# Kernel tuning notes

Hardware: AMD Instinct MI355X
Metric: run time of the kernel (lower is better)

The kernel has to match this reference:

```python
import jax, jax.numpy as jnp
import numpy as np

BATCH = 1024
SEQ = 80
VOCAB = 50000
EMB = 512
UNITS = 512


def setup_inputs() -> dict:
    key = jax.random.key(0)
    ks = jax.random.split(key, 10)
    s_in = 1.0 / np.sqrt(EMB)
    s_h = 1.0 / np.sqrt(UNITS)
    return {
        "inputs": jax.random.randint(ks[0], (BATCH, SEQ), 0, VOCAB, dtype=jnp.int64),
        "emb": jax.random.normal(ks[1], (VOCAB, EMB), dtype=jnp.float32) * 0.05,
        "W0x": jax.random.normal(ks[2], (EMB, UNITS), dtype=jnp.float32) * s_in,
        "W0h": jax.random.normal(ks[3], (UNITS, UNITS), dtype=jnp.float32) * s_h,
        "b0": jnp.zeros((UNITS,), dtype=jnp.float32),
        "W1x": jax.random.normal(ks[4], (UNITS, UNITS), dtype=jnp.float32) * s_h,
        "W1h": jax.random.normal(ks[5], (UNITS, UNITS), dtype=jnp.float32) * s_h,
        "b1": jnp.zeros((UNITS,), dtype=jnp.float32),
        "Wout": jax.random.normal(ks[6], (UNITS, 1), dtype=jnp.float32) * s_h,
        "bout": jnp.zeros((1,), dtype=jnp.float32),
    }


def reference(inputs, emb, W0x, W0h, b0, W1x, W1h, b1, Wout, bout):
    # Embedding lookup: [B, T, E]
    x = emb[inputs]
    # Time-major for scan: [T, B, E]
    xs = jnp.transpose(x, (1, 0, 2))

    h0 = jnp.zeros((inputs.shape[0], W0h.shape[0]), dtype=emb.dtype)
    h1 = jnp.zeros((inputs.shape[0], W1h.shape[0]), dtype=emb.dtype)

    def step(carry, x_t):
        h0, h1 = carry
        # SimpleRNNCell 0: tanh(x@Wx + h@Wh + b)  (dropout inactive at inference)
        h0 = jnp.tanh(x_t @ W0x + h0 @ W0h + b0)
        # SimpleRNNCell 1 stacked on cell 0's output
        h1 = jnp.tanh(h0 @ W1x + h1 @ W1h + b1)
        return (h0, h1), None

    (h0, h1), _ = jax.lax.scan(step, (h0, h1), xs)
    # Dense(1) on last-step hidden of layer 1, then sigmoid -> [B, 1]
    prob = jax.nn.sigmoid(h1 @ Wout + bout)
    return prob
```

## Files before the change

### kernel.cpp

```cpp
#include <hip/hip_runtime.h>
#include <hip/hip_bf16.h>
#include <math.h>

#define BATCH   1024
#define SEQ     80
#define EMB     512
#define UNITS   512
#define NBG     64
#define NCG     4
#define ROWS    16
#define COLS    128
#define THREADS 512
#define LDW     1544

#define H0_OFF   (2u * 1024 * 1024)
#define H1_OFF   (4u * 1024 * 1024)
#define FLAG_OFF (6u * 1024 * 1024)

typedef __attribute__((ext_vector_type(8))) short          bf16x8;
typedef __attribute__((ext_vector_type(8))) unsigned short u16x8;
typedef __attribute__((ext_vector_type(4))) float          f32x4;

__device__ inline unsigned short f2bf(float f) {
    __hip_bfloat16 h = __float2bfloat16(f);
    return *reinterpret_cast<unsigned short*>(&h);
}
__device__ inline float bf2f(unsigned short u) {
    unsigned int x = ((unsigned int)u) << 16;
    return __uint_as_float(x);
}
__device__ inline float tanh_fast(float x) {
    float e = __expf(2.f * x);
    return 1.f - 2.f / (e + 1.f);
}

__global__ __launch_bounds__(256) void pack_weights(
    const float* __restrict__ W0x, const float* __restrict__ W0h,
    const float* __restrict__ W1x, const float* __restrict__ W1h,
    unsigned short* __restrict__ wpack)
{
    int g    = blockIdx.x * 4 + (threadIdx.x >> 6);
    int lane = threadIdx.x & 63;
    int p    = g >> 10;
    int cg   = (g >> 8) & 3;
    int w    = (g >> 5) & 7;
    int k0   = g & 31;
    int n    = cg * COLS + w * 16 + (lane & 15);
    int kb   = k0 * 32 + (lane >> 4) * 8;
    const float* Wx = p ? W1x : W0x;
    const float* Wh = p ? W1h : W0h;

    u16x8 v;
#pragma unroll
    for (int j = 0; j < 8; ++j) {
        int k = kb + j;
        float f = (k < 512) ? Wx[(size_t)k * UNITS + n]
                            : Wh[(size_t)(k - 512) * UNITS + n];
        v[j] = f2bf(f);
    }
    *(u16x8*)(wpack + (size_t)g * 512 + lane * 8) = v;
}

#define RUN_PHASE(ACC, KBASE, WB)                                              \
    do {                                                                       \
        const unsigned short* a_lds = hcat + abase + (KBASE);                  \
        bf16x8 Bf[8];                                                          \
        _Pragma("unroll")                                                      \
        for (int i = 0; i < 8; ++i)                                            \
            Bf[i] = *(const bf16x8*)((WB) + (size_t)i * 512);                  \
        _Pragma("unroll")                                                      \
        for (int k0 = 0; k0 < 32; ++k0) {                                      \
            bf16x8 a = *(const bf16x8*)(a_lds + k0 * 32);                      \
            bf16x8 b = Bf[k0 & 7];                                             \
            if (k0 + 8 < 32)                                                   \
                Bf[k0 & 7] = *(const bf16x8*)((WB) + (size_t)(k0 + 8) * 512);  \
            ACC = __builtin_amdgcn_mfma_f32_16x16x32_bf16(a, b, ACC, 0, 0, 0); \
        }                                                                      \
    } while (0)

__global__ __launch_bounds__(THREADS, 1) void rnn_ex_kernel(
    const int*   __restrict__ inputs,
    const float* __restrict__ emb,
    const float* __restrict__ b0,
    const float* __restrict__ b1,
    const unsigned short* __restrict__ wpack,
    unsigned short* __restrict__ h0buf,
    unsigned short* __restrict__ h1buf,
    int* __restrict__ flag0,
    int* __restrict__ flag1,
    const float* __restrict__ Wout,
    const float* __restrict__ bout,
    float*       __restrict__ out)
{
    __shared__ unsigned short hcat[ROWS * LDW];

    const int tid   = threadIdx.x;
    const int w     = tid >> 6;
    const int lane  = tid & 63;
    const int quad  = lane >> 4;
    const int l15   = lane & 15;
    const int cg    = blockIdx.x >> 6;
    const int bg    = blockIdx.x & 63;
    const int rbase = bg * ROWS;

    for (int i = tid; i < ROWS * 1024; i += THREADS) {
        int r = i >> 10, c = i & 1023;
        hcat[r * LDW + 512 + c] = 0;
    }

    const int xr = tid >> 5;
    const int xc = (tid & 31) * 16;

    {
        int idx = inputs[(rbase + xr) * SEQ + 0];
        const float4* ep = (const float4*)(emb + (size_t)idx * EMB + xc);
        float4 p0 = ep[0], p1 = ep[1], p2 = ep[2], p3 = ep[3];
        u16x8 v0, v1;
        v0[0]=f2bf(p0.x); v0[1]=f2bf(p0.y); v0[2]=f2bf(p0.z); v0[3]=f2bf(p0.w);
        v0[4]=f2bf(p1.x); v0[5]=f2bf(p1.y); v0[6]=f2bf(p1.z); v0[7]=f2bf(p1.w);
        v1[0]=f2bf(p2.x); v1[1]=f2bf(p2.y); v1[2]=f2bf(p2.z); v1[3]=f2bf(p2.w);
        v1[4]=f2bf(p3.x); v1[5]=f2bf(p3.y); v1[6]=f2bf(p3.z); v1[7]=f2bf(p3.w);
        *(u16x8*)(hcat + xr * LDW + xc)     = v0;
        *(u16x8*)(hcat + xr * LDW + xc + 8) = v1;
    }
    __syncthreads();

    const int   mycol = cg * COLS + w * 16 + l15;
    const float bias0 = b0[mycol];
    const float bias1 = b1[mycol];

    const unsigned short* wb0 = wpack + ((size_t)(cg * 256 + w * 32)) * 512 + lane * 8;
    const unsigned short* wb1 = wb0 + (size_t)1024 * 512;

    const int abase = l15 * LDW + quad * 8;
    const int fl    = bg * NCG;

    for (int t = 0; t < SEQ; ++t) {
        const int par = t & 1;
        const int tgt = t + 1;

        int tn = (t + 1 < SEQ) ? t + 1 : t;
        int idx = inputs[(rbase + xr) * SEQ + tn];
        const float4* ep = (const float4*)(emb + (size_t)idx * EMB + xc);
        float4 p0 = ep[0], p1 = ep[1], p2 = ep[2], p3 = ep[3];

        f32x4 acc = {bias0, bias0, bias0, bias0};
        RUN_PHASE(acc, 0, wb0);
        {
            unsigned short* dst = h0buf +
                ((size_t)par * BATCH + rbase + quad * 4) * UNITS + mycol;
#pragma unroll
            for (int i = 0; i < 4; ++i)
                __hip_atomic_store(dst + (size_t)i * UNITS,
                                   f2bf(tanh_fast(acc[i])),
                                   __ATOMIC_RELAXED, __HIP_MEMORY_SCOPE_AGENT);
        }
        __syncthreads();
        if (tid == 0)
            __hip_atomic_store(&flag0[fl + cg], tgt,
                               __ATOMIC_RELEASE, __HIP_MEMORY_SCOPE_AGENT);
        if (tid < NCG)
            while (__hip_atomic_load(&flag0[fl + tid],
                                     __ATOMIC_RELAXED, __HIP_MEMORY_SCOPE_AGENT) < tgt)
                __builtin_amdgcn_s_sleep(1);
        __asm__ volatile("" ::: "memory");
        __syncthreads();
        {
            const unsigned long long* src = (const unsigned long long*)
                (h0buf + ((size_t)par * BATCH + rbase) * UNITS);
            int base = (xr * 512 + xc) >> 2;
            unsigned long long q0 = __hip_atomic_load(src + base + 0, __ATOMIC_RELAXED, __HIP_MEMORY_SCOPE_AGENT);
            unsigned long long q1 = __hip_atomic_load(src + base + 1, __ATOMIC_RELAXED, __HIP_MEMORY_SCOPE_AGENT);
            unsigned long long q2 = __hip_atomic_load(src + base + 2, __ATOMIC_RELAXED, __HIP_MEMORY_SCOPE_AGENT);
            unsigned long long q3 = __hip_atomic_load(src + base + 3, __ATOMIC_RELAXED, __HIP_MEMORY_SCOPE_AGENT);
            unsigned long long* d = (unsigned long long*)&hcat[xr * LDW + 512 + xc];
            d[0] = q0; d[1] = q1; d[2] = q2; d[3] = q3;

            u16x8 v0, v1;
            v0[0]=f2bf(p0.x); v0[1]=f2bf(p0.y); v0[2]=f2bf(p0.z); v0[3]=f2bf(p0.w);
            v0[4]=f2bf(p1.x); v0[5]=f2bf(p1.y); v0[6]=f2bf(p1.z); v0[7]=f2bf(p1.w);
            v1[0]=f2bf(p2.x); v1[1]=f2bf(p2.y); v1[2]=f2bf(p2.z); v1[3]=f2bf(p2.w);
            v1[4]=f2bf(p3.x); v1[5]=f2bf(p3.y); v1[6]=f2bf(p3.z); v1[7]=f2bf(p3.w);
            *(u16x8*)(hcat + xr * LDW + xc)     = v0;
            *(u16x8*)(hcat + xr * LDW + xc + 8) = v1;
        }
        __syncthreads();

        f32x4 acc2 = {bias1, bias1, bias1, bias1};
        RUN_PHASE(acc2, 512, wb1);
        {
            unsigned short* dst = h1buf +
                ((size_t)par * BATCH + rbase + quad * 4) * UNITS + mycol;
#pragma unroll
            for (int i = 0; i < 4; ++i)
                __hip_atomic_store(dst + (size_t)i * UNITS,
                                   f2bf(tanh_fast(acc2[i])),
                                   __ATOMIC_RELAXED, __HIP_MEMORY_SCOPE_AGENT);
        }
        __syncthreads();
        if (tid == 0)
            __hip_atomic_store(&flag1[fl + cg], tgt,
                               __ATOMIC_RELEASE, __HIP_MEMORY_SCOPE_AGENT);
        if (tid < NCG)
            while (__hip_atomic_load(&flag1[fl + tid],
                                     __ATOMIC_RELAXED, __HIP_MEMORY_SCOPE_AGENT) < tgt)
                __builtin_amdgcn_s_sleep(1);
        __asm__ volatile("" ::: "memory");
        __syncthreads();
        {
            const unsigned long long* src = (const unsigned long long*)
                (h1buf + ((size_t)par * BATCH + rbase) * UNITS);
            int base = (xr * 512 + xc) >> 2;
            unsigned long long q0 = __hip_atomic_load(src + base + 0, __ATOMIC_RELAXED, __HIP_MEMORY_SCOPE_AGENT);
            unsigned long long q1 = __hip_atomic_load(src + base + 1, __ATOMIC_RELAXED, __HIP_MEMORY_SCOPE_AGENT);
            unsigned long long q2 = __hip_atomic_load(src + base + 2, __ATOMIC_RELAXED, __HIP_MEMORY_SCOPE_AGENT);
            unsigned long long q3 = __hip_atomic_load(src + base + 3, __ATOMIC_RELAXED, __HIP_MEMORY_SCOPE_AGENT);
            unsigned long long* d = (unsigned long long*)&hcat[xr * LDW + 1024 + xc];
            d[0] = q0; d[1] = q1; d[2] = q2; d[3] = q3;
        }
    }
    __syncthreads();

    if (cg == 0) {
#pragma unroll
        for (int rr = 0; rr < 2; ++rr) {
            int r = w * 2 + rr;
            float s = 0.f;
#pragma unroll
            for (int j = 0; j < 8; ++j) {
                int c = lane + 64 * j;
                s += bf2f(hcat[r * LDW + 1024 + c]) * Wout[c];
            }
#pragma unroll
            for (int off = 32; off > 0; off >>= 1) s += __shfl_down(s, off);
            if (lane == 0) {
                float z = s + bout[0];
                out[rbase + r] = 1.f / (1.f + __expf(-z));
            }
        }
    }
}

extern "C" void kernel_launch(void* const* d_in, const int* in_sizes, int n_in,
                              void* d_out, int out_size, void* d_ws, size_t ws_size,
                              hipStream_t stream) {
    const int*   inputs = (const int*)d_in[0];
    const float* emb    = (const float*)d_in[1];
    const float* W0x    = (const float*)d_in[2];
    const float* W0h    = (const float*)d_in[3];
    const float* b0     = (const float*)d_in[4];
    const float* W1x    = (const float*)d_in[5];
    const float* W1h    = (const float*)d_in[6];
    const float* b1     = (const float*)d_in[7];
    const float* Wout   = (const float*)d_in[8];
    const float* bout   = (const float*)d_in[9];
    float*       out    = (float*)d_out;

    unsigned short* wpack = (unsigned short*)d_ws;
    unsigned short* h0buf = (unsigned short*)((char*)d_ws + H0_OFF);
    unsigned short* h1buf = (unsigned short*)((char*)d_ws + H1_OFF);
    int* flag0 = (int*)((char*)d_ws + FLAG_OFF);
    int* flag1 = flag0 + 256;

    hipMemsetAsync((char*)d_ws + FLAG_OFF, 0, 2048, stream);
    pack_weights<<<512, 256, 0, stream>>>(W0x, W0h, W1x, W1h, wpack);
    rnn_ex_kernel<<<NBG * NCG, THREADS, 0, stream>>>(
        inputs, emb, b0, b1, wpack, h0buf, h1buf, flag0, flag1,
        Wout, bout, out);
}
```

Before: 1.103 ms.

## Pipeline RNN as four producer/consumer stages over ring buffers per batch group

Splits the work by matrix instead of by output column: four block groups each own one of W0x, W0h, W1x, W1h, all 512 output columns. The input projection (stage 0) and the layer-1 input projection (stage 2) are taken off the recurrent critical path and pass results through 5-deep global ring buffers guarded by flags. The recurrent stages keep h in double-buffered LDS, so no cross-block exchange of h slices is needed. The cost is extra global traffic for fp32 partial sums, more flag polling, and a serial chain of dependent stages whose latency may still bound throughput.

Result: slower. 1.700 ms (+54.2%).

```diff
diff --git a/kernel.cpp b/kernel.cpp
--- a/kernel.cpp
+++ b/kernel.cpp
@@ -7,19 +7,15 @@
 #define EMB     512
 #define UNITS   512
 #define NBG     64
-#define NCG     4
 #define ROWS    16
-#define COLS    128
 #define THREADS 512
-#define LDW     1544
-
-#define H0_OFF   (2u * 1024 * 1024)
-#define H1_OFF   (4u * 1024 * 1024)
-#define FLAG_OFF (6u * 1024 * 1024)
-
-typedef __attribute__((ext_vector_type(8))) short          bf16x8;
-typedef __attribute__((ext_vector_type(8))) unsigned short u16x8;
-typedef __attribute__((ext_vector_type(4))) float          f32x4;
+#define RING    5
+#define LDH     520
+
+typedef __attribute__((ext_vector_type(8))) short              bf16x8;
+typedef __attribute__((ext_vector_type(8))) unsigned short     u16x8;
+typedef __attribute__((ext_vector_type(4))) float              f32x4;
+typedef __attribute__((ext_vector_type(2))) unsigned long long u64x2;
 
 __device__ inline unsigned short f2bf(float f) {
     __hip_bfloat16 h = __float2bfloat16(f);
@@ -32,6 +28,27 @@
 __device__ inline float tanh_fast(float x) {
     float e = __expf(2.f * x);
     return 1.f - 2.f / (e + 1.f);
+}
+__device__ inline u16x8 pack8(float4 p0, float4 p1) {
+    u16x8 v;
+    v[0]=f2bf(p0.x); v[1]=f2bf(p0.y); v[2]=f2bf(p0.z); v[3]=f2bf(p0.w);
+    v[4]=f2bf(p1.x); v[5]=f2bf(p1.y); v[6]=f2bf(p1.z); v[7]=f2bf(p1.w);
+    return v;
+}
+__device__ inline void st_f32(float* p, float v) {
+    __hip_atomic_store(p, v, __ATOMIC_RELAXED, __HIP_MEMORY_SCOPE_AGENT);
+}
+__device__ inline void st_u16(unsigned short* p, unsigned short v) {
+    __hip_atomic_store(p, v, __ATOMIC_RELAXED, __HIP_MEMORY_SCOPE_AGENT);
+}
+__device__ inline float ld_f32(const float* p) {
+    return __hip_atomic_load(p, __ATOMIC_RELAXED, __HIP_MEMORY_SCOPE_AGENT);
+}
+__device__ inline unsigned long long ld_u64(const unsigned long long* p) {
+    return __hip_atomic_load(p, __ATOMIC_RELAXED, __HIP_MEMORY_SCOPE_AGENT);
+}
+__device__ inline int ld_flag(const int* p) {
+    return __hip_atomic_load(p, __ATOMIC_RELAXED, __HIP_MEMORY_SCOPE_AGENT);
 }
 
 __global__ __launch_bounds__(256) void pack_weights(
@@ -41,187 +58,260 @@
 {
     int g    = blockIdx.x * 4 + (threadIdx.x >> 6);
     int lane = threadIdx.x & 63;
-    int p    = g >> 10;
-    int cg   = (g >> 8) & 3;
-    int w    = (g >> 5) & 7;
-    int k0   = g & 31;
-    int n    = cg * COLS + w * 16 + (lane & 15);
-    int kb   = k0 * 32 + (lane >> 4) * 8;
-    const float* Wx = p ? W1x : W0x;
-    const float* Wh = p ? W1h : W0h;
+    int m    = g >> 9;
+    int w    = (g >> 6) & 7;
+    int nt   = (g >> 4) & 3;
+    int k    = g & 15;
+    int col  = w * 64 + nt * 16 + (lane & 15);
+    int rowb = k * 32 + (lane >> 4) * 8;
+    const float* src = (m == 0) ? W0x : (m == 1) ? W0h : (m == 2) ? W1x : W1h;
 
     u16x8 v;
 #pragma unroll
-    for (int j = 0; j < 8; ++j) {
-        int k = kb + j;
-        float f = (k < 512) ? Wx[(size_t)k * UNITS + n]
-                            : Wh[(size_t)(k - 512) * UNITS + n];
-        v[j] = f2bf(f);
-    }
+    for (int j = 0; j < 8; ++j)
+        v[j] = f2bf(src[(size_t)(rowb + j) * UNITS + col]);
     *(u16x8*)(wpack + (size_t)g * 512 + lane * 8) = v;
 }
 
-#define RUN_PHASE(ACC, KBASE, WB)                                              \
+#define NT_GEMM(ACC, WN)                                                       \
     do {                                                                       \
-        const unsigned short* a_lds = hcat + abase + (KBASE);                  \
-        bf16x8 Bf[8];                                                          \
+        bf16x8 Bf_[8];                                                         \
         _Pragma("unroll")                                                      \
-        for (int i = 0; i < 8; ++i)                                            \
-            Bf[i] = *(const bf16x8*)((WB) + (size_t)i * 512);                  \
+        for (int i_ = 0; i_ < 8; ++i_)                                         \
+            Bf_[i_] = *(const bf16x8*)((WN) + (size_t)i_ * 512);               \
         _Pragma("unroll")                                                      \
-        for (int k0 = 0; k0 < 32; ++k0) {                                      \
-            bf16x8 a = *(const bf16x8*)(a_lds + k0 * 32);                      \
-            bf16x8 b = Bf[k0 & 7];                                             \
-            if (k0 + 8 < 32)                                                   \
-                Bf[k0 & 7] = *(const bf16x8*)((WB) + (size_t)(k0 + 8) * 512);  \
-            ACC = __builtin_amdgcn_mfma_f32_16x16x32_bf16(a, b, ACC, 0, 0, 0); \
+        for (int k_ = 0; k_ < 16; ++k_) {                                      \
+            bf16x8 b_ = Bf_[k_ & 7];                                           \
+            if (k_ + 8 < 16)                                                   \
+                Bf_[k_ & 7] = *(const bf16x8*)((WN) + (size_t)(k_ + 8) * 512); \
+            ACC = __builtin_amdgcn_mfma_f32_16x16x32_bf16(av[k_], b_, ACC,     \
+                                                          0, 0, 0);            \
         }                                                                      \
     } while (0)
 
-__global__ __launch_bounds__(THREADS, 1) void rnn_ex_kernel(
+__global__ __launch_bounds__(THREADS, 2) void rnn_pipe(
     const int*   __restrict__ inputs,
     const float* __restrict__ emb,
     const float* __restrict__ b0,
     const float* __restrict__ b1,
     const unsigned short* __restrict__ wpack,
-    unsigned short* __restrict__ h0buf,
-    unsigned short* __restrict__ h1buf,
-    int* __restrict__ flag0,
-    int* __restrict__ flag1,
+    float*          __restrict__ pxring,
+    unsigned short* __restrict__ h0ring,
+    float*          __restrict__ uring,
+    int*            __restrict__ flg,
     const float* __restrict__ Wout,
     const float* __restrict__ bout,
     float*       __restrict__ out)
 {
-    __shared__ unsigned short hcat[ROWS * LDW];
+    __shared__ __align__(16) unsigned short sA[2 * ROWS * LDH];
 
     const int tid   = threadIdx.x;
     const int w     = tid >> 6;
     const int lane  = tid & 63;
     const int quad  = lane >> 4;
     const int l15   = lane & 15;
-    const int cg    = blockIdx.x >> 6;
+    const int stage = blockIdx.x >> 6;
     const int bg    = blockIdx.x & 63;
     const int rbase = bg * ROWS;
 
-    for (int i = tid; i < ROWS * 1024; i += THREADS) {
-        int r = i >> 10, c = i & 1023;
-        hcat[r * LDW + 512 + c] = 0;
-    }
-
-    const int xr = tid >> 5;
-    const int xc = (tid & 31) * 16;
-
-    {
-        int idx = inputs[(rbase + xr) * SEQ + 0];
-        const float4* ep = (const float4*)(emb + (size_t)idx * EMB + xc);
-        float4 p0 = ep[0], p1 = ep[1], p2 = ep[2], p3 = ep[3];
-        u16x8 v0, v1;
-        v0[0]=f2bf(p0.x); v0[1]=f2bf(p0.y); v0[2]=f2bf(p0.z); v0[3]=f2bf(p0.w);
-        v0[4]=f2bf(p1.x); v0[5]=f2bf(p1.y); v0[6]=f2bf(p1.z); v0[7]=f2bf(p1.w);
-        v1[0]=f2bf(p2.x); v1[1]=f2bf(p2.y); v1[2]=f2bf(p2.z); v1[3]=f2bf(p2.w);
-        v1[4]=f2bf(p3.x); v1[5]=f2bf(p3.y); v1[6]=f2bf(p3.z); v1[7]=f2bf(p3.w);
-        *(u16x8*)(hcat + xr * LDW + xc)     = v0;
-        *(u16x8*)(hcat + xr * LDW + xc + 8) = v1;
-    }
-    __syncthreads();
-
-    const int   mycol = cg * COLS + w * 16 + l15;
-    const float bias0 = b0[mycol];
-    const float bias1 = b1[mycol];
-
-    const unsigned short* wb0 = wpack + ((size_t)(cg * 256 + w * 32)) * 512 + lane * 8;
-    const unsigned short* wb1 = wb0 + (size_t)1024 * 512;
-
-    const int abase = l15 * LDW + quad * 8;
-    const int fl    = bg * NCG;
-
-    for (int t = 0; t < SEQ; ++t) {
-        const int par = t & 1;
-        const int tgt = t + 1;
-
-        int tn = (t + 1 < SEQ) ? t + 1 : t;
-        int idx = inputs[(rbase + xr) * SEQ + tn];
-        const float4* ep = (const float4*)(emb + (size_t)idx * EMB + xc);
-        float4 p0 = ep[0], p1 = ep[1], p2 = ep[2], p3 = ep[3];
-
-        f32x4 acc = {bias0, bias0, bias0, bias0};
-        RUN_PHASE(acc, 0, wb0);
-        {
-            unsigned short* dst = h0buf +
-                ((size_t)par * BATCH + rbase + quad * 4) * UNITS + mycol;
-#pragma unroll
-            for (int i = 0; i < 4; ++i)
-                __hip_atomic_store(dst + (size_t)i * UNITS,
-                                   f2bf(tanh_fast(acc[i])),
-                                   __ATOMIC_RELAXED, __HIP_MEMORY_SCOPE_AGENT);
+    const int gr   = w;
+    const int gc   = lane * 8;
+    const int aoff = l15 * LDH + quad * 8;
+    const int col0 = w * 64 + l15;
+
+    int* Fpx = flg;
+    int* Fh0 = flg + 64;
+    int* Fu  = flg + 128;
+    int* Fh1 = flg + 192;
+
+    const unsigned short* wb = wpack + ((size_t)((stage * 8 + w) * 64)) * 512
+                                     + lane * 8;
+
+    if (stage == 0) {
+        float bb[4];
+#pragma unroll
+        for (int nt = 0; nt < 4; ++nt) bb[nt] = b0[col0 + nt * 16];
+
+        for (int t = 0; t < SEQ; ++t) {
+            if (tid == 0)
+                while (ld_flag(&Fh0[bg]) < t - (RING - 1))
+                    __builtin_amdgcn_s_sleep(1);
+            __asm__ volatile("" ::: "memory");
+            __syncthreads();
+            if (tid == 0)
+                __hip_atomic_store(&Fpx[bg], t, __ATOMIC_RELEASE,
+                                   __HIP_MEMORY_SCOPE_AGENT);
+            {
+                int ia = inputs[(rbase + gr) * SEQ + t];
+                int ib = inputs[(rbase + gr + 8) * SEQ + t];
+                const float4* ea = (const float4*)(emb + (size_t)ia * EMB + gc);
+                const float4* eb = (const float4*)(emb + (size_t)ib * EMB + gc);
+                float4 f0 = ea[0], f1 = ea[1], f2 = eb[0], f3 = eb[1];
+                *(u16x8*)(sA + gr * LDH + gc)       = pack8(f0, f1);
+                *(u16x8*)(sA + (gr + 8) * LDH + gc) = pack8(f2, f3);
+            }
+            __syncthreads();
+
+            bf16x8 av[16];
+            const unsigned short* ar = sA + aoff;
+#pragma unroll
+            for (int k = 0; k < 16; ++k) av[k] = *(const bf16x8*)(ar + k * 32);
+
+            f32x4 acc[4];
+#pragma unroll
+            for (int nt = 0; nt < 4; ++nt) {
+                acc[nt] = (f32x4){bb[nt], bb[nt], bb[nt], bb[nt]};
+                NT_GEMM(acc[nt], wb + (size_t)(nt * 16) * 512);
+            }
+            float* dst = pxring + ((size_t)(t % RING) * NBG + bg) * 8192;
+#pragma unroll
+            for (int nt = 0; nt < 4; ++nt)
+#pragma unroll
+                for (int i = 0; i < 4; ++i)
+                    st_f32(dst + (quad * 4 + i) * 512 + col0 + nt * 16,
+                           acc[nt][i]);
         }
         __syncthreads();
         if (tid == 0)
-            __hip_atomic_store(&flag0[fl + cg], tgt,
-                               __ATOMIC_RELEASE, __HIP_MEMORY_SCOPE_AGENT);
-        if (tid < NCG)
-            while (__hip_atomic_load(&flag0[fl + tid],
-                                     __ATOMIC_RELAXED, __HIP_MEMORY_SCOPE_AGENT) < tgt)
-                __builtin_amdgcn_s_sleep(1);
-        __asm__ volatile("" ::: "memory");
-        __syncthreads();
-        {
-            const unsigned long long* src = (const unsigned long long*)
-                (h0buf + ((size_t)par * BATCH + rbase) * UNITS);
-            int base = (xr * 512 + xc) >> 2;
-            unsigned long long q0 = __hip_atomic_load(src + base + 0, __ATOMIC_RELAXED, __HIP_MEMORY_SCOPE_AGENT);
-            unsigned long long q1 = __hip_atomic_load(src + base + 1, __ATOMIC_RELAXED, __HIP_MEMORY_SCOPE_AGENT);
-            unsigned long long q2 = __hip_atomic_load(src + base + 2, __ATOMIC_RELAXED, __HIP_MEMORY_SCOPE_AGENT);
-            unsigned long long q3 = __hip_atomic_load(src + base + 3, __ATOMIC_RELAXED, __HIP_MEMORY_SCOPE_AGENT);
-            unsigned long long* d = (unsigned long long*)&hcat[xr * LDW + 512 + xc];
-            d[0] = q0; d[1] = q1; d[2] = q2; d[3] = q3;
-
-            u16x8 v0, v1;
-            v0[0]=f2bf(p0.x); v0[1]=f2bf(p0.y); v0[2]=f2bf(p0.z); v0[3]=f2bf(p0.w);
-            v0[4]=f2bf(p1.x); v0[5]=f2bf(p1.y); v0[6]=f2bf(p1.z); v0[7]=f2bf(p1.w);
-            v1[0]=f2bf(p2.x); v1[1]=f2bf(p2.y); v1[2]=f2bf(p2.z); v1[3]=f2bf(p2.w);
-            v1[4]=f2bf(p3.x); v1[5]=f2bf(p3.y); v1[6]=f2bf(p3.z); v1[7]=f2bf(p3.w);
-            *(u16x8*)(hcat + xr * LDW + xc)     = v0;
-            *(u16x8*)(hcat + xr * LDW + xc + 8) = v1;
-        }
-        __syncthreads();
-
-        f32x4 acc2 = {bias1, bias1, bias1, bias1};
-        RUN_PHASE(acc2, 512, wb1);
-        {
-            unsigned short* dst = h1buf +
-                ((size_t)par * BATCH + rbase + quad * 4) * UNITS + mycol;
-#pragma unroll
-            for (int i = 0; i < 4; ++i)
-                __hip_atomic_store(dst + (size_t)i * UNITS,
-                                   f2bf(tanh_fast(acc2[i])),
-                                   __ATOMIC_RELAXED, __HIP_MEMORY_SCOPE_AGENT);
+            __hip_atomic_store(&Fpx[bg], SEQ + 1, __ATOMIC_RELEASE,
+                               __HIP_MEMORY_SCOPE_AGENT);
+
+    } else if (stage == 1) {
+        for (int i = tid; i < ROWS * LDH; i += THREADS)
+            sA[ROWS * LDH + i] = 0;
+
+        for (int t = 0; t < SEQ; ++t) {
+            const int par = t & 1, slot = t % RING;
+            if (tid == 0) {
+                while (ld_flag(&Fu[bg])  < t - (RING - 1)) __builtin_amdgcn_s_sleep(1);
+                while (ld_flag(&Fpx[bg]) < t + 1)          __builtin_amdgcn_s_sleep(1);
+            }
+            __asm__ volatile("" ::: "memory");
+            __syncthreads();
+            if (tid == 0)
+                __hip_atomic_store(&Fh0[bg], t, __ATOMIC_RELEASE,
+                                   __HIP_MEMORY_SCOPE_AGENT);
+            const float* ps = pxring + ((size_t)slot * NBG + bg) * 8192;
+            f32x4 acc[4];
+#pragma unroll
+            for (int nt = 0; nt < 4; ++nt)
+#pragma unroll
+                for (int i = 0; i < 4; ++i)
+                    acc[nt][i] = ld_f32(ps + (quad * 4 + i) * 512 + col0 + nt * 16);
+
+            bf16x8 av[16];
+            const unsigned short* ar = sA + (par ^ 1) * ROWS * LDH + aoff;
+#pragma unroll
+            for (int k = 0; k < 16; ++k) av[k] = *(const bf16x8*)(ar + k * 32);
+#pragma unroll
+            for (int nt = 0; nt < 4; ++nt)
+                NT_GEMM(acc[nt], wb + (size_t)(nt * 16) * 512);
+
+            unsigned short* hd = sA + par * ROWS * LDH;
+            unsigned short* rs = h0ring + ((size_t)slot * NBG + bg) * 8192;
+#pragma unroll
+            for (int nt = 0; nt < 4; ++nt)
+#pragma unroll
+                for (int i = 0; i < 4; ++i) {
+                    unsigned short hv = f2bf(tanh_fast(acc[nt][i]));
+                    hd[(quad * 4 + i) * LDH + col0 + nt * 16] = hv;
+                    st_u16(rs + (quad * 4 + i) * 512 + col0 + nt * 16, hv);
+                }
         }
         __syncthreads();
         if (tid == 0)
-            __hip_atomic_store(&flag1[fl + cg], tgt,
-                               __ATOMIC_RELEASE, __HIP_MEMORY_SCOPE_AGENT);
-        if (tid < NCG)
-            while (__hip_atomic_load(&flag1[fl + tid],
-                                     __ATOMIC_RELAXED, __HIP_MEMORY_SCOPE_AGENT) < tgt)
-                __builtin_amdgcn_s_sleep(1);
-        __asm__ volatile("" ::: "memory");
+            __hip_atomic_store(&Fh0[bg], SEQ + 1, __ATOMIC_RELEASE,
+                               __HIP_MEMORY_SCOPE_AGENT);
+
+    } else if (stage == 2) {
+        float bb[4];
+#pragma unroll
+        for (int nt = 0; nt < 4; ++nt) bb[nt] = b1[col0 + nt * 16];
+
+        for (int t = 0; t < SEQ; ++t) {
+            const int slot = t % RING;
+            if (tid == 0) {
+                while (ld_flag(&Fh1[bg]) < t - (RING - 1)) __builtin_amdgcn_s_sleep(1);
+                while (ld_flag(&Fh0[bg]) < t + 1)          __builtin_amdgcn_s_sleep(1);
+            }
+            __asm__ volatile("" ::: "memory");
+            __syncthreads();
+            if (tid == 0)
+                __hip_atomic_store(&Fu[bg], t, __ATOMIC_RELEASE,
+                                   __HIP_MEMORY_SCOPE_AGENT);
+            const unsigned long long* hs = (const unsigned long long*)
+                (h0ring + ((size_t)slot * NBG + bg) * 8192);
+            bf16x8 av[16];
+#pragma unroll
+            for (int k = 0; k < 16; ++k) {
+                int eo = l15 * 512 + k * 32 + quad * 8;
+                u64x2 q;
+                q[0] = ld_u64(hs + (eo >> 2));
+                q[1] = ld_u64(hs + (eo >> 2) + 1);
+                av[k] = *(bf16x8*)&q;
+            }
+            f32x4 acc[4];
+#pragma unroll
+            for (int nt = 0; nt < 4; ++nt) {
+                acc[nt] = (f32x4){bb[nt], bb[nt], bb[nt], bb[nt]};
+                NT_GEMM(acc[nt], wb + (size_t)(nt * 16) * 512);
+            }
+            float* dst = uring + ((size_t)slot * NBG + bg) * 8192;
+#pragma unroll
+            for (int nt = 0; nt < 4; ++nt)
+#pragma unroll
+                for (int i = 0; i < 4; ++i)
+                    st_f32(dst + (quad * 4 + i) * 512 + col0 + nt * 16,
+                           acc[nt][i]);
+        }
         __syncthreads();
-        {
-            const unsigned long long* src = (const unsigned long long*)
-                (h1buf + ((size_t)par * BATCH + rbase) * UNITS);
-            int base = (xr * 512 + xc) >> 2;
-            unsigned long long q0 = __hip_atomic_load(src + base + 0, __ATOMIC_RELAXED, __HIP_MEMORY_SCOPE_AGENT);
-            unsigned long long q1 = __hip_atomic_load(src + base + 1, __ATOMIC_RELAXED, __HIP_MEMORY_SCOPE_AGENT);
-            unsigned long long q2 = __hip_atomic_load(src + base + 2, __ATOMIC_RELAXED, __HIP_MEMORY_SCOPE_AGENT);
-            unsigned long long q3 = __hip_atomic_load(src + base + 3, __ATOMIC_RELAXED, __HIP_MEMORY_SCOPE_AGENT);
-            unsigned long long* d = (unsigned long long*)&hcat[xr * LDW + 1024 + xc];
-            d[0] = q0; d[1] = q1; d[2] = q2; d[3] = q3;
-        }
-    }
-    __syncthreads();
-
-    if (cg == 0) {
+        if (tid == 0)
+            __hip_atomic_store(&Fu[bg], SEQ + 1, __ATOMIC_RELEASE,
+                               __HIP_MEMORY_SCOPE_AGENT);
+
+    } else {
+        for (int i = tid; i < ROWS * LDH; i += THREADS)
+            sA[ROWS * LDH + i] = 0;
+
+        for (int t = 0; t < SEQ; ++t) {
+            const int par = t & 1, slot = t % RING;
+            if (tid == 0)
+                while (ld_flag(&Fu[bg]) < t + 1) __builtin_amdgcn_s_sleep(1);
+            __asm__ volatile("" ::: "memory");
+            __syncthreads();
+            if (tid == 0)
+                __hip_atomic_store(&Fh1[bg], t, __ATOMIC_RELEASE,
+                                   __HIP_MEMORY_SCOPE_AGENT);
+            const float* us = uring + ((size_t)slot * NBG + bg) * 8192;
+            f32x4 acc[4];
+#pragma unroll
+            for (int nt = 0; nt < 4; ++nt)
+#pragma unroll
+                for (int i = 0; i < 4; ++i)
+                    acc[nt][i] = ld_f32(us + (quad * 4 + i) * 512 + col0 + nt * 16);
+
+            bf16x8 av[16];
+            const unsigned short* ar = sA + (par ^ 1) * ROWS * LDH + aoff;
+#pragma unroll
+            for (int k = 0; k < 16; ++k) av[k] = *(const bf16x8*)(ar + k * 32);
+#pragma unroll
+            for (int nt = 0; nt < 4; ++nt)
+                NT_GEMM(acc[nt], wb + (size_t)(nt * 16) * 512);
+
+            unsigned short* hd = sA + par * ROWS * LDH;
+#pragma unroll
+            for (int nt = 0; nt < 4; ++nt)
+#pragma unroll
+                for (int i = 0; i < 4; ++i)
+                    hd[(quad * 4 + i) * LDH + col0 + nt * 16] =
+                        f2bf(tanh_fast(acc[nt][i]));
+        }
+        __syncthreads();
+        if (tid == 0)
+            __hip_atomic_store(&Fh1[bg], SEQ + 1, __ATOMIC_RELEASE,
+                               __HIP_MEMORY_SCOPE_AGENT);
+
+        const unsigned short* h1l = sA + ((SEQ - 1) & 1) * ROWS * LDH;
 #pragma unroll
         for (int rr = 0; rr < 2; ++rr) {
             int r = w * 2 + rr;
@@ -229,7 +319,7 @@
 #pragma unroll
             for (int j = 0; j < 8; ++j) {
                 int c = lane + 64 * j;
-                s += bf2f(hcat[r * LDW + 1024 + c]) * Wout[c];
+                s += bf2f(h1l[r * LDH + c]) * Wout[c];
             }
 #pragma unroll
             for (int off = 32; off > 0; off >>= 1) s += __shfl_down(s, off);
@@ -256,15 +346,22 @@
     const float* bout   = (const float*)d_in[9];
     float*       out    = (float*)d_out;
 
-    unsigned short* wpack = (unsigned short*)d_ws;
-    unsigned short* h0buf = (unsigned short*)((char*)d_ws + H0_OFF);
-    unsigned short* h1buf = (unsigned short*)((char*)d_ws + H1_OFF);
-    int* flag0 = (int*)((char*)d_ws + FLAG_OFF);
-    int* flag1 = flag0 + 256;
-
-    hipMemsetAsync((char*)d_ws + FLAG_OFF, 0, 2048, stream);
+    char* base = (char*)d_ws;
+    const size_t WP_OFF = 0;
+    const size_t PX_OFF = (size_t)2  * 1024 * 1024;
+    const size_t H0_OFF = PX_OFF + (size_t)RING * 2097152;
+    const size_t U_OFF  = H0_OFF + (size_t)RING * 1048576;
+    const size_t FL_OFF = U_OFF  + (size_t)RING * 2097152;
+
+    unsigned short* wpack  = (unsigned short*)(base + WP_OFF);
+    float*          pxring = (float*)(base + PX_OFF);
+    unsigned short* h0ring = (unsigned short*)(base + H0_OFF);
+    float*          uring  = (float*)(base + U_OFF);
+    int*            flg    = (int*)(base + FL_OFF);
+
+    hipMemsetAsync(flg, 0, 2048, stream);
     pack_weights<<<512, 256, 0, stream>>>(W0x, W0h, W1x, W1h, wpack);
-    rnn_ex_kernel<<<NBG * NCG, THREADS, 0, stream>>>(
-        inputs, emb, b0, b1, wpack, h0buf, h1buf, flag0, flag1,
+    rnn_pipe<<<4 * NBG, THREADS, 0, stream>>>(
+        inputs, emb, b0, b1, wpack, pxring, h0ring, uring, flg,
         Wout, bout, out);
 }
```

## Split RNN layers across block groups with LDS-resident weights and layer pipelining

Applied to the files above, without the earlier changes.

Replaces the single kernel where every block runs both layers in lockstep with a layer-split design. 128 blocks compute layer 0 and 128 compute layer 1, so layer 1 at step t can overlap layer 0 at step t+1. Each block owns a 64-column by 64-row tile and keeps its weight slice resident in LDS instead of streaming it from global memory every step. The x-projection for the next step is computed off the critical path, and hidden states are staged through a small LDS ring buffer. In exchange there are more per-step __syncthreads inside the gather loops, cross-layer flag dependencies, and extra memsets to zero the initial hidden-state buffers.

Result: slower. 1.277 ms (+15.9%).

```diff
diff --git a/kernel.cpp b/kernel.cpp
--- a/kernel.cpp
+++ b/kernel.cpp
@@ -6,20 +6,18 @@
 #define SEQ     80
 #define EMB     512
 #define UNITS   512
-#define NBG     64
-#define NCG     4
-#define ROWS    16
-#define COLS    128
+#define NBG     16
+#define NJ      8
 #define THREADS 512
-#define LDW     1544
-
-#define H0_OFF   (2u * 1024 * 1024)
-#define H1_OFF   (4u * 1024 * 1024)
-#define FLAG_OFF (6u * 1024 * 1024)
-
-typedef __attribute__((ext_vector_type(8))) short          bf16x8;
-typedef __attribute__((ext_vector_type(8))) unsigned short u16x8;
-typedef __attribute__((ext_vector_type(4))) float          f32x4;
+
+#define H0_OFF (2u * 1024 * 1024)
+#define H1_OFF (4u * 1024 * 1024)
+#define FL_OFF (6u * 1024 * 1024)
+
+typedef __attribute__((ext_vector_type(8))) short              bf16x8;
+typedef __attribute__((ext_vector_type(8))) unsigned short     u16x8;
+typedef __attribute__((ext_vector_type(4))) float              f32x4;
+typedef __attribute__((ext_vector_type(2))) unsigned long long u64x2;
 
 __device__ inline unsigned short f2bf(float f) {
     __hip_bfloat16 h = __float2bfloat16(f);
@@ -32,6 +30,21 @@
 __device__ inline float tanh_fast(float x) {
     float e = __expf(2.f * x);
     return 1.f - 2.f / (e + 1.f);
+}
+__device__ inline u16x8 pack8(float4 p0, float4 p1) {
+    u16x8 v;
+    v[0]=f2bf(p0.x); v[1]=f2bf(p0.y); v[2]=f2bf(p0.z); v[3]=f2bf(p0.w);
+    v[4]=f2bf(p1.x); v[5]=f2bf(p1.y); v[6]=f2bf(p1.z); v[7]=f2bf(p1.w);
+    return v;
+}
+__device__ inline void st_u16(unsigned short* p, unsigned short v) {
+    __hip_atomic_store(p, v, __ATOMIC_RELAXED, __HIP_MEMORY_SCOPE_AGENT);
+}
+__device__ inline unsigned long long ld_u64(const unsigned long long* p) {
+    return __hip_atomic_load(p, __ATOMIC_RELAXED, __HIP_MEMORY_SCOPE_AGENT);
+}
+__device__ inline int ld_flag(const int* p) {
+    return __hip_atomic_load(p, __ATOMIC_RELAXED, __HIP_MEMORY_SCOPE_AGENT);
 }
 
 __global__ __launch_bounds__(256) void pack_weights(
@@ -41,44 +54,95 @@
 {
     int g    = blockIdx.x * 4 + (threadIdx.x >> 6);
     int lane = threadIdx.x & 63;
-    int p    = g >> 10;
-    int cg   = (g >> 8) & 3;
-    int w    = (g >> 5) & 7;
-    int k0   = g & 31;
-    int n    = cg * COLS + w * 16 + (lane & 15);
-    int kb   = k0 * 32 + (lane >> 4) * 8;
-    const float* Wx = p ? W1x : W0x;
-    const float* Wh = p ? W1h : W0h;
+    int type = g >> 10;
+    int j    = (g >> 7) & 7;
+    int mat  = (g >> 6) & 1;
+    int kk   = (g >> 2) & 15;
+    int nt   = g & 3;
+    const float* M = type ? (mat ? W1h : W1x) : (mat ? W0h : W0x);
+    int col  = j * 64 + nt * 16 + (lane & 15);
+    int rowb = kk * 32 + (lane >> 4) * 8;
 
     u16x8 v;
 #pragma unroll
-    for (int j = 0; j < 8; ++j) {
-        int k = kb + j;
-        float f = (k < 512) ? Wx[(size_t)k * UNITS + n]
-                            : Wh[(size_t)(k - 512) * UNITS + n];
-        v[j] = f2bf(f);
-    }
+    for (int jj = 0; jj < 8; ++jj)
+        v[jj] = f2bf(M[(size_t)(rowb + jj) * UNITS + col]);
     *(u16x8*)(wpack + (size_t)g * 512 + lane * 8) = v;
 }
 
-#define RUN_PHASE(ACC, KBASE, WB)                                              \
+#define WLD(mat, kk, nt)            ((((mat)*16 + (kk))*4 + (nt)) * 512)
+#define RNG(slot, kkl, row, quad)   (((((slot)*2 + (kkl))*64 + (row))*4 + (quad)) * 8)
+
+#define GATHER_GEMM(HB, PAR, MAT, A0, A1)                                      \
     do {                                                                       \
-        const unsigned short* a_lds = hcat + abase + (KBASE);                  \
-        bf16x8 Bf[8];                                                          \
-        _Pragma("unroll")                                                      \
-        for (int i = 0; i < 8; ++i)                                            \
-            Bf[i] = *(const bf16x8*)((WB) + (size_t)i * 512);                  \
-        _Pragma("unroll")                                                      \
-        for (int k0 = 0; k0 < 32; ++k0) {                                      \
-            bf16x8 a = *(const bf16x8*)(a_lds + k0 * 32);                      \
-            bf16x8 b = Bf[k0 & 7];                                             \
-            if (k0 + 8 < 32)                                                   \
-                Bf[k0 & 7] = *(const bf16x8*)((WB) + (size_t)(k0 + 8) * 512);  \
-            ACC = __builtin_amdgcn_mfma_f32_16x16x32_bf16(a, b, ACC, 0, 0, 0); \
+        const unsigned long long* hs_ = (const unsigned long long*)            \
+            ((HB) + ((size_t)(PAR) * BATCH + rbase) * UNITS);                  \
+        const int go_ = grow * 128 + gk8 * 2;                                  \
+        u64x2 ld_[8];                                                          \
+        _Pragma("unroll")                                                      \
+        for (int s_ = 0; s_ < 3; ++s_) {                                       \
+            ld_[s_][0] = ld_u64(hs_ + go_ + s_ * 16);                          \
+            ld_[s_][1] = ld_u64(hs_ + go_ + s_ * 16 + 1);                      \
+        }                                                                      \
+        _Pragma("unroll")                                                      \
+        for (int s_ = 0; s_ < 8; ++s_) {                                       \
+            *(u64x2*)(ring + RNG(s_ & 1, gk8 >> 2, grow, gk8 & 3)) = ld_[s_];  \
+            __syncthreads();                                                   \
+            if (s_ + 3 < 8) {                                                  \
+                ld_[s_+3][0] = ld_u64(hs_ + go_ + (s_+3) * 16);                \
+                ld_[s_+3][1] = ld_u64(hs_ + go_ + (s_+3) * 16 + 1);            \
+            }                                                                  \
+            _Pragma("unroll")                                                  \
+            for (int kl_ = 0; kl_ < 2; ++kl_) {                                \
+                bf16x8 a_ = *(const bf16x8*)(ring + RNG(s_ & 1, kl_, arow, quad)); \
+                int kg_ = s_ * 2 + kl_;                                        \
+                A0 = __builtin_amdgcn_mfma_f32_16x16x32_bf16(a_,               \
+                    *(const bf16x8*)(wlds + WLD(MAT, kg_, nt0) + lane*8), A0, 0,0,0); \
+                A1 = __builtin_amdgcn_mfma_f32_16x16x32_bf16(a_,               \
+                    *(const bf16x8*)(wlds + WLD(MAT, kg_, nt1) + lane*8), A1, 0,0,0); \
+            }                                                                  \
         }                                                                      \
     } while (0)
 
-__global__ __launch_bounds__(THREADS, 1) void rnn_ex_kernel(
+#define XSTAGE_GEMM(TT, A0, A1)                                                \
+    do {                                                                       \
+        int t_   = (TT) < SEQ ? (TT) : SEQ - 1;                                \
+        int idx_ = inputs[(rbase + grow) * SEQ + t_];                          \
+        const float4* ep_ = (const float4*)(emb + (size_t)idx_ * EMB) + gk8*2; \
+        float4 pa_[8], pb_[8];                                                 \
+        _Pragma("unroll")                                                      \
+        for (int s_ = 0; s_ < 3; ++s_) { pa_[s_] = ep_[s_*16]; pb_[s_] = ep_[s_*16+1]; } \
+        _Pragma("unroll")                                                      \
+        for (int s_ = 0; s_ < 8; ++s_) {                                       \
+            *(u16x8*)(ring + RNG(s_ & 1, gk8 >> 2, grow, gk8 & 3)) =           \
+                pack8(pa_[s_], pb_[s_]);                                       \
+            __syncthreads();                                                   \
+            if (s_ + 3 < 8) { pa_[s_+3] = ep_[(s_+3)*16]; pb_[s_+3] = ep_[(s_+3)*16+1]; } \
+            _Pragma("unroll")                                                  \
+            for (int kl_ = 0; kl_ < 2; ++kl_) {                                \
+                bf16x8 a_ = *(const bf16x8*)(ring + RNG(s_ & 1, kl_, arow, quad)); \
+                int kg_ = s_ * 2 + kl_;                                        \
+                A0 = __builtin_amdgcn_mfma_f32_16x16x32_bf16(a_,               \
+                    *(const bf16x8*)(wlds + WLD(0, kg_, nt0) + lane*8), A0, 0,0,0); \
+                A1 = __builtin_amdgcn_mfma_f32_16x16x32_bf16(a_,               \
+                    *(const bf16x8*)(wlds + WLD(0, kg_, nt1) + lane*8), A1, 0,0,0); \
+            }                                                                  \
+        }                                                                      \
+    } while (0)
+
+#define PUBLISH(HB, PAR, A0, A1)                                               \
+    do {                                                                       \
+        unsigned short* d_ = (HB) +                                            \
+            ((size_t)(PAR) * BATCH + rbase + rg * 16 + quad * 4) * UNITS       \
+            + c0 + l15;                                                        \
+        _Pragma("unroll")                                                      \
+        for (int i_ = 0; i_ < 4; ++i_) {                                       \
+            st_u16(d_ + (size_t)i_ * UNITS + nt0 * 16, f2bf(tanh_fast(A0[i_]))); \
+            st_u16(d_ + (size_t)i_ * UNITS + nt1 * 16, f2bf(tanh_fast(A1[i_]))); \
+        }                                                                      \
+    } while (0)
+
+__global__ __launch_bounds__(THREADS, 1) void rnn_ls(
     const int*   __restrict__ inputs,
     const float* __restrict__ emb,
     const float* __restrict__ b0,
@@ -92,150 +156,118 @@
     const float* __restrict__ bout,
     float*       __restrict__ out)
 {
-    __shared__ unsigned short hcat[ROWS * LDW];
+    __shared__ __align__(16) unsigned short wlds[2 * 16 * 4 * 512];
+    __shared__ __align__(16) unsigned short ring[2 * 2 * 64 * 4 * 8];
 
     const int tid   = threadIdx.x;
     const int w     = tid >> 6;
     const int lane  = tid & 63;
     const int quad  = lane >> 4;
     const int l15   = lane & 15;
-    const int cg    = blockIdx.x >> 6;
-    const int bg    = blockIdx.x & 63;
-    const int rbase = bg * ROWS;
-
-    for (int i = tid; i < ROWS * 1024; i += THREADS) {
-        int r = i >> 10, c = i & 1023;
-        hcat[r * LDW + 512 + c] = 0;
-    }
-
-    const int xr = tid >> 5;
-    const int xc = (tid & 31) * 16;
+    const int type  = blockIdx.x >> 7;
+    const int bidx  = blockIdx.x & 127;
+    const int bg    = bidx >> 3;
+    const int j     = bidx & 7;
+    const int rbase = bg * 64;
+    const int c0    = j * 64;
+
+    const int rg   = w >> 1;
+    const int ntp  = w & 1;
+    const int nt0  = 2 * ntp, nt1 = nt0 + 1;
+    const int arow = rg * 16 + l15;
+    const int grow = tid >> 3;
+    const int gk8  = tid & 7;
 
     {
-        int idx = inputs[(rbase + xr) * SEQ + 0];
-        const float4* ep = (const float4*)(emb + (size_t)idx * EMB + xc);
-        float4 p0 = ep[0], p1 = ep[1], p2 = ep[2], p3 = ep[3];
-        u16x8 v0, v1;
-        v0[0]=f2bf(p0.x); v0[1]=f2bf(p0.y); v0[2]=f2bf(p0.z); v0[3]=f2bf(p0.w);
-        v0[4]=f2bf(p1.x); v0[5]=f2bf(p1.y); v0[6]=f2bf(p1.z); v0[7]=f2bf(p1.w);
-        v1[0]=f2bf(p2.x); v1[1]=f2bf(p2.y); v1[2]=f2bf(p2.z); v1[3]=f2bf(p2.w);
-        v1[4]=f2bf(p3.x); v1[5]=f2bf(p3.y); v1[6]=f2bf(p3.z); v1[7]=f2bf(p3.w);
-        *(u16x8*)(hcat + xr * LDW + xc)     = v0;
-        *(u16x8*)(hcat + xr * LDW + xc + 8) = v1;
+        const unsigned short* wsrc = wpack + (size_t)(type * 8 + j) * 128 * 512;
+#pragma unroll
+        for (int i = 0; i < 16; ++i)
+            *(u16x8*)(wlds + (size_t)(i * 512 + tid) * 8) =
+                *(const u16x8*)(wsrc + (size_t)(i * 512 + tid) * 8);
     }
     __syncthreads();
 
-    const int   mycol = cg * COLS + w * 16 + l15;
-    const float bias0 = b0[mycol];
-    const float bias1 = b1[mycol];
-
-    const unsigned short* wb0 = wpack + ((size_t)(cg * 256 + w * 32)) * 512 + lane * 8;
-    const unsigned short* wb1 = wb0 + (size_t)1024 * 512;
-
-    const int abase = l15 * LDW + quad * 8;
-    const int fl    = bg * NCG;
-
-    for (int t = 0; t < SEQ; ++t) {
-        const int par = t & 1;
-        const int tgt = t + 1;
-
-        int tn = (t + 1 < SEQ) ? t + 1 : t;
-        int idx = inputs[(rbase + xr) * SEQ + tn];
-        const float4* ep = (const float4*)(emb + (size_t)idx * EMB + xc);
-        float4 p0 = ep[0], p1 = ep[1], p2 = ep[2], p3 = ep[3];
-
-        f32x4 acc = {bias0, bias0, bias0, bias0};
-        RUN_PHASE(acc, 0, wb0);
-        {
-            unsigned short* dst = h0buf +
-                ((size_t)par * BATCH + rbase + quad * 4) * UNITS + mycol;
-#pragma unroll
-            for (int i = 0; i < 4; ++i)
-                __hip_atomic_store(dst + (size_t)i * UNITS,
-                                   f2bf(tanh_fast(acc[i])),
-                                   __ATOMIC_RELAXED, __HIP_MEMORY_SCOPE_AGENT);
+    const float* bp   = type ? b1 : b0;
+    const float  bia0 = bp[c0 + nt0 * 16 + l15];
+    const float  bia1 = bp[c0 + nt1 * 16 + l15];
+
+    if (type == 0) {
+        f32x4 aX0 = {bia0, bia0, bia0, bia0};
+        f32x4 aX1 = {bia1, bia1, bia1, bia1};
+        XSTAGE_GEMM(0, aX0, aX1);
+
+        for (int r = 0; r < SEQ; ++r) {
+            const int par = r & 1;
+            if (tid < 8)
+                while (ld_flag(flag0 + bg * 8 + tid) < r)
+                    __builtin_amdgcn_s_sleep(1);
+            else if (tid < 16)
+                while (ld_flag(flag1 + bg * 8 + (tid - 8)) < r - 1)
+                    __builtin_amdgcn_s_sleep(1);
+            __asm__ volatile("" ::: "memory");
+            __syncthreads();
+
+            f32x4 a0 = aX0, a1 = aX1;
+            GATHER_GEMM(h0buf, par ^ 1, 1, a0, a1);
+            PUBLISH(h0buf, par, a0, a1);
+            __syncthreads();
+            if (tid == 0)
+                __hip_atomic_store(flag0 + bg * 8 + j, r + 1,
+                                   __ATOMIC_RELEASE, __HIP_MEMORY_SCOPE_AGENT);
+
+            aX0 = (f32x4){bia0, bia0, bia0, bia0};
+            aX1 = (f32x4){bia1, bia1, bia1, bia1};
+            XSTAGE_GEMM(r + 1, aX0, aX1);
         }
-        __syncthreads();
-        if (tid == 0)
-            __hip_atomic_store(&flag0[fl + cg], tgt,
-                               __ATOMIC_RELEASE, __HIP_MEMORY_SCOPE_AGENT);
-        if (tid < NCG)
-            while (__hip_atomic_load(&flag0[fl + tid],
-                                     __ATOMIC_RELAXED, __HIP_MEMORY_SCOPE_AGENT) < tgt)
-                __builtin_amdgcn_s_sleep(1);
-        __asm__ volatile("" ::: "memory");
-        __syncthreads();
-        {
-            const unsigned long long* src = (const unsigned long long*)
-                (h0buf + ((size_t)par * BATCH + rbase) * UNITS);
-            int base = (xr * 512 + xc) >> 2;
-            unsigned long long q0 = __hip_atomic_load(src + base + 0, __ATOMIC_RELAXED, __HIP_MEMORY_SCOPE_AGENT);
-            unsigned long long q1 = __hip_atomic_load(src + base + 1, __ATOMIC_RELAXED, __HIP_MEMORY_SCOPE_AGENT);
-            unsigned long long q2 = __hip_atomic_load(src + base + 2, __ATOMIC_RELAXED, __HIP_MEMORY_SCOPE_AGENT);
-            unsigned long long q3 = __hip_atomic_load(src + base + 3, __ATOMIC_RELAXED, __HIP_MEMORY_SCOPE_AGENT);
-            unsigned long long* d = (unsigned long long*)&hcat[xr * LDW + 512 + xc];
-            d[0] = q0; d[1] = q1; d[2] = q2; d[3] = q3;
-
-            u16x8 v0, v1;
-            v0[0]=f2bf(p0.x); v0[1]=f2bf(p0.y); v0[2]=f2bf(p0.z); v0[3]=f2bf(p0.w);
-            v0[4]=f2bf(p1.x); v0[5]=f2bf(p1.y); v0[6]=f2bf(p1.z); v0[7]=f2bf(p1.w);
-            v1[0]=f2bf(p2.x); v1[1]=f2bf(p2.y); v1[2]=f2bf(p2.z); v1[3]=f2bf(p2.w);
-            v1[4]=f2bf(p3.x); v1[5]=f2bf(p3.y); v1[6]=f2bf(p3.z); v1[7]=f2bf(p3.w);
-            *(u16x8*)(hcat + xr * LDW + xc)     = v0;
-            *(u16x8*)(hcat + xr * LDW + xc + 8) = v1;
+    } else {
+        for (int s = 0; s < SEQ; ++s) {
+            const int par = s & 1;
+            if (tid < 8)
+                while (ld_flag(flag0 + bg * 8 + tid) < s + 1)
+                    __builtin_amdgcn_s_sleep(1);
+            else if (tid < 16)
+                while (ld_flag(flag1 + bg * 8 + (tid - 8)) < s)
+                    __builtin_amdgcn_s_sleep(1);
+            __asm__ volatile("" ::: "memory");
+            __syncthreads();
+
+            f32x4 a0 = {bia0, bia0, bia0, bia0};
+            f32x4 a1 = {bia1, bia1, bia1, bia1};
+            GATHER_GEMM(h0buf, par,     0, a0, a1);
+            GATHER_GEMM(h1buf, par ^ 1, 1, a0, a1);
+            PUBLISH(h1buf, par, a0, a1);
+            __syncthreads();
+            if (tid == 0)
+                __hip_atomic_store(flag1 + bg * 8 + j, s + 1,
+                                   __ATOMIC_RELEASE, __HIP_MEMORY_SCOPE_AGENT);
         }
-        __syncthreads();
-
-        f32x4 acc2 = {bias1, bias1, bias1, bias1};
-        RUN_PHASE(acc2, 512, wb1);
-        {
-            unsigned short* dst = h1buf +
-                ((size_t)par * BATCH + rbase + quad * 4) * UNITS + mycol;
-#pragma unroll
-            for (int i = 0; i < 4; ++i)
-                __hip_atomic_store(dst + (size_t)i * UNITS,
-                                   f2bf(tanh_fast(acc2[i])),
-                                   __ATOMIC_RELAXED, __HIP_MEMORY_SCOPE_AGENT);
-        }
-        __syncthreads();
-        if (tid == 0)
-            __hip_atomic_store(&flag1[fl + cg], tgt,
-                               __ATOMIC_RELEASE, __HIP_MEMORY_SCOPE_AGENT);
-        if (tid < NCG)
-            while (__hip_atomic_load(&flag1[fl + tid],
-                                     __ATOMIC_RELAXED, __HIP_MEMORY_SCOPE_AGENT) < tgt)
-                __builtin_amdgcn_s_sleep(1);
-        __asm__ volatile("" ::: "memory");
-        __syncthreads();
-        {
-            const unsigned long long* src = (const unsigned long long*)
-                (h1buf + ((size_t)par * BATCH + rbase) * UNITS);
-            int base = (xr * 512 + xc) >> 2;
-            unsigned long long q0 = __hip_atomic_load(src + base + 0, __ATOMIC_RELAXED, __HIP_MEMORY_SCOPE_AGENT);
-            unsigned long long q1 = __hip_atomic_load(src + base + 1, __ATOMIC_RELAXED, __HIP_MEMORY_SCOPE_AGENT);
-            unsigned long long q2 = __hip_atomic_load(src + base + 2, __ATOMIC_RELAXED, __HIP_MEMORY_SCOPE_AGENT);
-            unsigned long long q3 = __hip_atomic_load(src + base + 3, __ATOMIC_RELAXED, __HIP_MEMORY_SCOPE_AGENT);
-            unsigned long long* d = (unsigned long long*)&hcat[xr * LDW + 1024 + xc];
-            d[0] = q0; d[1] = q1; d[2] = q2; d[3] = q3;
-        }
-    }
-    __syncthreads();
-
-    if (cg == 0) {
-#pragma unroll
-        for (int rr = 0; rr < 2; ++rr) {
-            int r = w * 2 + rr;
-            float s = 0.f;
-#pragma unroll
-            for (int j = 0; j < 8; ++j) {
-                int c = lane + 64 * j;
-                s += bf2f(hcat[r * LDW + 1024 + c]) * Wout[c];
-            }
-#pragma unroll
-            for (int off = 32; off > 0; off >>= 1) s += __shfl_down(s, off);
-            if (lane == 0) {
-                float z = s + bout[0];
-                out[rbase + r] = 1.f / (1.f + __expf(-z));
+
+        if (j == 0) {
+            if (tid < 8)
+                while (ld_flag(flag1 + bg * 8 + tid) < SEQ)
+                    __builtin_amdgcn_s_sleep(1);
+            __asm__ volatile("" ::: "memory");
+            __syncthreads();
+            const unsigned long long* hs = (const unsigned long long*)
+                (h1buf + ((size_t)((SEQ - 1) & 1) * BATCH + rbase) * UNITS);
+#pragma unroll
+            for (int i = 0; i < 8; ++i) {
+                int row = w * 8 + i;
+                unsigned long long q0 = ld_u64(hs + row * 128 + lane * 2);
+                unsigned long long q1 = ld_u64(hs + row * 128 + lane * 2 + 1);
+                u64x2 qq; qq[0] = q0; qq[1] = q1;
+                u16x8 hv = *(u16x8*)&qq;
+                float sacc = 0.f;
+#pragma unroll
+                for (int k = 0; k < 8; ++k)
+                    sacc += bf2f(hv[k]) * Wout[lane * 8 + k];
+#pragma unroll
+                for (int off = 32; off > 0; off >>= 1)
+                    sacc += __shfl_down(sacc, off);
+                if (lane == 0) {
+                    float z = sacc + bout[0];
+                    out[rbase + row] = 1.f / (1.f + __expf(-z));
+                }
             }
         }
     }
@@ -259,12 +291,16 @@
     unsigned short* wpack = (unsigned short*)d_ws;
     unsigned short* h0buf = (unsigned short*)((char*)d_ws + H0_OFF);
     unsigned short* h1buf = (unsigned short*)((char*)d_ws + H1_OFF);
-    int* flag0 = (int*)((char*)d_ws + FLAG_OFF);
-    int* flag1 = flag0 + 256;
-
-    hipMemsetAsync((char*)d_ws + FLAG_OFF, 0, 2048, stream);
+    int* flag0 = (int*)((char*)d_ws + FL_OFF);
+    int* flag1 = flag0 + 128;
+
+    hipMemsetAsync((char*)d_ws + FL_OFF, 0, 1024, stream);
+    hipMemsetAsync((char*)h0buf + (size_t)BATCH * UNITS * 2, 0,
+                   (size_t)BATCH * UNITS * 2, stream);
+    hipMemsetAsync((char*)h1buf + (size_t)BATCH * UNITS * 2, 0,
+                   (size_t)BATCH * UNITS * 2, stream);
     pack_weights<<<512, 256, 0, stream>>>(W0x, W0h, W1x, W1h, wpack);
-    rnn_ex_kernel<<<NBG * NCG, THREADS, 0, stream>>>(
+    rnn_ls<<<256, THREADS, 0, stream>>>(
         inputs, emb, b0, b1, wpack, h0buf, h1buf, flag0, flag1,
         Wout, bout, out);
 }
```
